# Optimization experiments

Measured on AMD Instinct MI355X. Metric: run time of the kernel, lower is better.

## Reference

```python
import jax, jax.numpy as jnp
import numpy as np

T, B, E = 1024, 4, 1024
H = 16
D = E // H          # head_dim = 64
L = 16              # max_relative_length


def setup_inputs() -> dict:
    key = jax.random.key(0)
    ks = jax.random.split(key, 4)
    query = jax.random.normal(ks[0], (T, B, E), dtype=jnp.float32)
    # xavier-ish scaled params
    in_proj_weight = jax.random.normal(ks[1], (3 * E, E), dtype=jnp.float32) * (1.0 / np.sqrt(E))
    in_proj_bias = jnp.zeros((3 * E,), dtype=jnp.float32)
    rel_pos_keys = jax.random.normal(ks[2], (2 * L + 1, E), dtype=jnp.float32) * (1.0 / np.sqrt(E))
    out_w = jax.random.normal(ks[3], (E, E), dtype=jnp.float32) * (1.0 / np.sqrt(E))
    out_b = jnp.zeros((E,), dtype=jnp.float32)
    return {"query": query, "in_proj_weight": in_proj_weight, "in_proj_bias": in_proj_bias,
            "rel_pos_keys": rel_pos_keys, "out_w": out_w, "out_b": out_b}


def reference(query, in_proj_weight, in_proj_bias, rel_pos_keys, out_w, out_b):
    t, b, e = query.shape
    scaling = D ** (-0.5)
    # fused qkv projection: [T,B,3E]
    qkv = jnp.einsum('tbe,fe->tbf', query, in_proj_weight) + in_proj_bias
    q, k, v = jnp.split(qkv, 3, axis=-1)
    q = q * scaling
    # [T,B,E] -> [B*H, T, D]
    def heads(x):
        return x.reshape(t, b * H, D).transpose(1, 0, 2)
    q, k, v = heads(q), heads(k), heads(v)
    # clipped relative position matrix [T,T] in [0, 2L]
    r = jnp.arange(t)
    dist = jnp.clip(r[None, :] - r[:, None], -L, L) + L
    # gather relation keys, keep first head_dim channels: [T,T,D]
    rel_k = rel_pos_keys[dist][:, :, :D]
    # scores = q k^T + q . rel_k  (Shaw et al.), [B*H, T, T]
    scores = jnp.einsum('btd,bsd->bts', q, k) + jnp.einsum('btd,tsd->bts', q, rel_k)
    probs = jax.nn.softmax(scores, axis=-1)
    attn = jnp.einsum('bts,bsd->btd', probs, v)      # [B*H, T, D]
    attn = attn.transpose(1, 0, 2).reshape(t, b, e)   # [T, B, E]
    return jnp.einsum('tbe,oe->tbo', attn, out_w) + out_b
```

## Files before the change

### kernel.cpp

```cpp
#include <hip/hip_runtime.h>

typedef __attribute__((ext_vector_type(8))) short short8;
typedef __attribute__((ext_vector_type(4))) float floatx4;


__device__ __forceinline__ short f2bf(float x) {
  union { float f; unsigned u; } cv; cv.f = x;
  unsigned u = cv.u + (0x7FFFu + ((cv.u >> 16) & 1u));
  return (short)(u >> 16);
}

__device__ __forceinline__ floatx4 mfma16(short8 a, short8 b, floatx4 c) {
  return __builtin_amdgcn_mfma_f32_16x16x32_bf16(a, b, c, 0, 0, 0);
}

__device__ __forceinline__ void async_copy16(const void* g, void* l) {
  __builtin_amdgcn_global_load_lds((const __attribute__((address_space(1))) void*)g,
                                   (__attribute__((address_space(3))) void*)l, 16, 0, 0);
}

__global__ void __launch_bounds__(256) f32_to_bf16_kernel(
    const float* __restrict__ src, short* __restrict__ dst, int n8)
{
  int i = blockIdx.x * 256 + threadIdx.x;
  if (i >= n8) return;
  const float4* s = (const float4*)src;
  float4 a = s[i * 2], b = s[i * 2 + 1];
  short8 o;
  o[0] = f2bf(a.x); o[1] = f2bf(a.y); o[2] = f2bf(a.z); o[3] = f2bf(a.w);
  o[4] = f2bf(b.x); o[5] = f2bf(b.y); o[6] = f2bf(b.z); o[7] = f2bf(b.w);
  *(short8*)(dst + (size_t)i * 8) = o;
}

__device__ __forceinline__ void gemm_core(
    const short* __restrict__ A, const short* __restrict__ W,
    short* Atile, short* Btile,
    int m0, int n0, int K, int tid, floatx4 acc[4][4])
{
  const int lane = tid & 63, w = tid >> 6;
  const int quad = lane >> 4, l16 = lane & 15;
  const int wm = (w >> 1) * 64, wn = (w & 1) * 64;
  #pragma unroll
  for (int mt = 0; mt < 4; mt++)
    #pragma unroll
    for (int nt = 0; nt < 4; nt++) acc[mt][nt] = (floatx4)(0.0f);

  for (int kk = 0; kk < K; kk += 32) {
    #pragma unroll
    for (int i = 0; i < 2; i++) {
      int seg = i * 256 + tid;
      int row = seg >> 2, c = seg & 3;
      const short* gA = A + (size_t)(m0 + row) * K + kk + c * 8;
      const short* gB = W + (size_t)(n0 + row) * K + kk + c * 8;
      async_copy16(gA, Atile + (size_t)(i * 256 + w * 64) * 8);
      async_copy16(gB, Btile + (size_t)(i * 256 + w * 64) * 8);
    }
    __syncthreads();
    short8 af[4], bfr[4];
    #pragma unroll
    for (int mt = 0; mt < 4; mt++)
      af[mt] = *(const short8*)(Atile + (wm + mt * 16 + l16) * 32 + quad * 8);
    #pragma unroll
    for (int nt = 0; nt < 4; nt++)
      bfr[nt] = *(const short8*)(Btile + (wn + nt * 16 + l16) * 32 + quad * 8);
    #pragma unroll
    for (int mt = 0; mt < 4; mt++)
      #pragma unroll
      for (int nt = 0; nt < 4; nt++)
        acc[mt][nt] = mfma16(af[mt], bfr[nt], acc[mt][nt]);
    __syncthreads();
  }
}

__global__ void __launch_bounds__(256) gemm_qkv(
    const short* __restrict__ A, const short* __restrict__ W,
    const float* __restrict__ bias,
    short* __restrict__ q_ws, short* __restrict__ k_ws, short* __restrict__ v_ws)
{
  __shared__ __align__(16) short Atile[128 * 32];
  __shared__ __align__(16) short Btile[128 * 32];
  const int tid = threadIdx.x;
  const int m0 = blockIdx.x * 128, n0 = blockIdx.y * 128;
  floatx4 acc[4][4];
  gemm_core(A, W, Atile, Btile, m0, n0, 1024, tid, acc);

  const int lane = tid & 63, w = tid >> 6;
  const int quad = lane >> 4, l16 = lane & 15;
  const int wm = (w >> 1) * 64, wn = (w & 1) * 64;
  #pragma unroll
  for (int nt = 0; nt < 4; nt++) {
    int f = n0 + wn + nt * 16 + l16;
    float bv = bias[f];
    int which = f >> 10;
    int h = (f >> 6) & 15;
    int d = f & 63;
    #pragma unroll
    for (int mt = 0; mt < 4; mt++) {
      #pragma unroll
      for (int reg = 0; reg < 4; reg++) {
        int r = m0 + wm + mt * 16 + quad * 4 + reg;
        int t = r >> 2, b = r & 3;
        int bh = b * 16 + h;
        float val = acc[mt][nt][reg] + bv;
        if (which == 0)      q_ws[((size_t)bh * 1024 + t) * 64 + d] = f2bf(val * 0.125f);
        else if (which == 1) k_ws[((size_t)bh * 1024 + t) * 64 + d] = f2bf(val);
        else                 v_ws[((size_t)bh * 64 + d) * 1024 + t] = f2bf(val);
      }
    }
  }
}

__global__ void __launch_bounds__(256) attn_kernel(
    const short* __restrict__ q_ws, const short* __restrict__ k_ws,
    const short* __restrict__ v_ws, const float* __restrict__ relk,
    short* __restrict__ attn_ws)
{
  __shared__ float rel_lds[64 * 33];
  __shared__ __align__(16) short Ktile[64 * 64];
  __shared__ __align__(16) short Vtile[64 * 64];
  __shared__ __align__(16) short p_lds[4][16 * 64];
  const int tid = threadIdx.x, lane = tid & 63, w = tid >> 6;
  const int quad = lane >> 4, l16 = lane & 15;
  const int bh = blockIdx.x >> 4;
  const int t0 = (blockIdx.x & 15) * 64;
  const int b = bh >> 4, h = bh & 15;

  short8 aq[2];
  #pragma unroll
  for (int ks = 0; ks < 2; ks++)
    aq[ks] = *(const short8*)(q_ws + ((size_t)bh * 1024 + t0 + w * 16 + l16) * 64
                              + ks * 32 + quad * 8);

  for (int i = tid; i < 48 * 8; i += 256) {
    int row = i >> 3, p = i & 7;
    short8 val;
    if (row < 33) {
      const float* src = relk + row * 1024 + p * 8;
      float4 a = *(const float4*)src, c = *(const float4*)(src + 4);
      val[0] = f2bf(a.x); val[1] = f2bf(a.y); val[2] = f2bf(a.z); val[3] = f2bf(a.w);
      val[4] = f2bf(c.x); val[5] = f2bf(c.y); val[6] = f2bf(c.z); val[7] = f2bf(c.w);
    } else {
      val = (short8)0;
    }
    *(short8*)(Ktile + row * 64 + ((p ^ (row & 7)) << 3)) = val;
  }
  __syncthreads();

  #pragma unroll
  for (int jt = 0; jt < 3; jt++) {
    floatx4 scR = (floatx4)(0.0f);
    #pragma unroll
    for (int ks = 0; ks < 2; ks++) {
      int rrow = jt * 16 + l16;
      int ck = (quad + 4 * ks) ^ (rrow & 7);
      short8 rb = *(const short8*)(Ktile + rrow * 64 + ck * 8);
      scR = mfma16(aq[ks], rb, scR);
    }
    int j = jt * 16 + l16;
    if (j < 33) {
      #pragma unroll
      for (int reg = 0; reg < 4; reg++) {
        int tl = w * 16 + quad * 4 + reg;
        rel_lds[tl * 33 + j] = scR[reg];
      }
    }
  }
  __syncthreads();

  floatx4 o[4];
  #pragma unroll
  for (int dt = 0; dt < 4; dt++) o[dt] = (floatx4)(0.0f);
  float rsum[4] = {0.f, 0.f, 0.f, 0.f};

  float biasLo[4], biasHi[4];
  #pragma unroll
  for (int reg = 0; reg < 4; reg++) {
    int tl = w * 16 + quad * 4 + reg;
    biasLo[reg] = rel_lds[tl * 33 + 0];
    biasHi[reg] = rel_lds[tl * 33 + 32];
  }

  const short* kg = k_ws + (size_t)bh * 1024 * 64;
  const short* vg = v_ws + (size_t)bh * 64 * 1024;

  for (int st = 0; st < 16; st++) {
    const int s0 = st * 64;
    #pragma unroll
    for (int i = 0; i < 2; i++) {
      int seg = i * 256 + tid;
      int row = seg >> 3, p = seg & 7;
      int ck = p ^ (row & 7);
      async_copy16(kg + (size_t)(s0 + row) * 64 + ck * 8,
                   Ktile + (size_t)(i * 256 + w * 64) * 8);
      async_copy16(vg + (size_t)row * 1024 + s0 + ck * 8,
                   Vtile + (size_t)(i * 256 + w * 64) * 8);
    }
    __syncthreads();

    floatx4 sc[4];
    #pragma unroll
    for (int nt = 0; nt < 4; nt++) {
      sc[nt] = (floatx4)(0.0f);
      #pragma unroll
      for (int ks = 0; ks < 2; ks++) {
        int srow = nt * 16 + l16;
        int ck = (quad + 4 * ks) ^ (l16 & 7);
        short8 kb = *(const short8*)(Ktile + srow * 64 + ck * 8);
        sc[nt] = mfma16(aq[ks], kb, sc[nt]);
      }
    }

    bool alllo = (s0 <= t0 + w * 16 - 79);
    bool allhi = (s0 >= t0 + w * 16 + 31);
    if (alllo || allhi) {
      #pragma unroll
      for (int reg = 0; reg < 4; reg++) {
        float bb = alllo ? biasLo[reg] : biasHi[reg];
        #pragma unroll
        for (int nt = 0; nt < 4; nt++) sc[nt][reg] += bb;
      }
    } else {
      #pragma unroll
      for (int nt = 0; nt < 4; nt++) {
        int s_glob = s0 + nt * 16 + l16;
        #pragma unroll
        for (int reg = 0; reg < 4; reg++) {
          int tl = w * 16 + quad * 4 + reg;
          int delta = min(max(s_glob - (t0 + tl), -16), 16) + 16;
          sc[nt][reg] += rel_lds[tl * 33 + delta];
        }
      }
    }

    #pragma unroll
    for (int nt = 0; nt < 4; nt++)
      #pragma unroll
      for (int reg = 0; reg < 4; reg++) {
        float p = __expf(sc[nt][reg]);
        sc[nt][reg] = p;
        rsum[reg] += p;
      }

    #pragma unroll
    for (int nt = 0; nt < 4; nt++)
      #pragma unroll
      for (int reg = 0; reg < 4; reg++) {
        int r = quad * 4 + reg;
        int cg = 2 * nt + (l16 >> 3);
        p_lds[w][r * 64 + ((cg ^ (r & 7)) << 3) + (l16 & 7)] = f2bf(sc[nt][reg]);
      }
    short8 ap[2];
    #pragma unroll
    for (int ks = 0; ks < 2; ks++) {
      int ck = (quad + 4 * ks) ^ (l16 & 7);
      ap[ks] = *(const short8*)(&p_lds[w][l16 * 64 + ck * 8]);
    }

    #pragma unroll
    for (int dt = 0; dt < 4; dt++) {
      #pragma unroll
      for (int ks = 0; ks < 2; ks++) {
        int drow = dt * 16 + l16;
        int ck = (quad + 4 * ks) ^ (l16 & 7);
        short8 vb = *(const short8*)(Vtile + drow * 64 + ck * 8);
        o[dt] = mfma16(ap[ks], vb, o[dt]);
      }
    }
    __syncthreads();
  }

  #pragma unroll
  for (int reg = 0; reg < 4; reg++) {
    float rs = rsum[reg];
    #pragma unroll
    for (int off = 1; off < 16; off <<= 1) rs += __shfl_xor(rs, off, 64);
    rsum[reg] = 1.0f / rs;
  }
  #pragma unroll
  for (int dt = 0; dt < 4; dt++) {
    #pragma unroll
    for (int reg = 0; reg < 4; reg++) {
      int tg = t0 + w * 16 + quad * 4 + reg;
      attn_ws[((size_t)tg * 4 + b) * 1024 + h * 64 + dt * 16 + l16]
        = f2bf(o[dt][reg] * rsum[reg]);
    }
  }
}

__global__ void __launch_bounds__(256) gemm_outproj(
    const short* __restrict__ A, const short* __restrict__ W,
    const float* __restrict__ bias, float* __restrict__ out)
{
  __shared__ __align__(16) short Atile[128 * 32];
  __shared__ __align__(16) short Btile[128 * 32];
  const int tid = threadIdx.x;
  const int m0 = blockIdx.x * 128, n0 = blockIdx.y * 128;
  floatx4 acc[4][4];
  gemm_core(A, W, Atile, Btile, m0, n0, 1024, tid, acc);

  const int lane = tid & 63, w = tid >> 6;
  const int quad = lane >> 4, l16 = lane & 15;
  const int wm = (w >> 1) * 64, wn = (w & 1) * 64;
  #pragma unroll
  for (int nt = 0; nt < 4; nt++) {
    int f = n0 + wn + nt * 16 + l16;
    float bv = bias[f];
    #pragma unroll
    for (int mt = 0; mt < 4; mt++) {
      #pragma unroll
      for (int reg = 0; reg < 4; reg++) {
        int r = m0 + wm + mt * 16 + quad * 4 + reg;
        out[(size_t)r * 1024 + f] = acc[mt][nt][reg] + bv;
      }
    }
  }
}

extern "C" void kernel_launch(void* const* d_in, const int* in_sizes, int n_in,
                              void* d_out, int out_size, void* d_ws, size_t ws_size,
                              hipStream_t stream) {
  const float* query = (const float*)d_in[0];
  const float* in_w  = (const float*)d_in[1];
  const float* in_b  = (const float*)d_in[2];
  const float* relk  = (const float*)d_in[3];
  const float* out_w = (const float*)d_in[4];
  const float* out_b = (const float*)d_in[5];
  float* out = (float*)d_out;

  short* qry_bf = (short*)d_ws;
  short* win_bf = qry_bf + (size_t)4096 * 1024;
  short* wout_bf = win_bf + (size_t)3072 * 1024;
  short* q_ws   = wout_bf + (size_t)1024 * 1024;
  short* k_ws   = q_ws + (size_t)64 * 1024 * 64;
  short* v_ws   = k_ws + (size_t)64 * 1024 * 64;
  short* att_ws = v_ws + (size_t)64 * 1024 * 64;

  f32_to_bf16_kernel<<<4096 * 1024 / 8 / 256, 256, 0, stream>>>(query, qry_bf, 4096 * 1024 / 8);
  f32_to_bf16_kernel<<<3072 * 1024 / 8 / 256, 256, 0, stream>>>(in_w, win_bf, 3072 * 1024 / 8);
  f32_to_bf16_kernel<<<1024 * 1024 / 8 / 256, 256, 0, stream>>>(out_w, wout_bf, 1024 * 1024 / 8);

  gemm_qkv<<<dim3(32, 24), 256, 0, stream>>>(qry_bf, win_bf, in_b, q_ws, k_ws, v_ws);
  attn_kernel<<<1024, 256, 0, stream>>>(q_ws, k_ws, v_ws, relk, att_ws);
  gemm_outproj<<<dim3(32, 8), 256, 0, stream>>>(att_ws, wout_bf, out_b, out);
}
```

Before: 198.0 us.

## Double-buffer LDS tiles in GEMMs and attention to overlap loads with MFMA

Splits the GEMM and attention K/V tile buffers into two LDS stages and issues the next tile's async global-to-LDS copy right after the barrier, before computing on the current tile. It also drops the trailing barrier in each loop. The goal is to hide global memory latency behind MFMA work. This doubles LDS use per block, which may reduce occupancy. Nothing explicitly waits for the async LDS loads (vmcnt) before the barrier, so correctness relies on how the barrier and the compiler order those loads.

```diff
diff --git a/kernel.cpp b/kernel.cpp
--- a/kernel.cpp
+++ b/kernel.cpp
@@ -32,9 +32,24 @@
   *(short8*)(dst + (size_t)i * 8) = o;
 }
 
-__device__ __forceinline__ void gemm_core(
+__device__ __forceinline__ void gemm_stage(
     const short* __restrict__ A, const short* __restrict__ W,
-    short* Atile, short* Btile,
+    short* Atile, short* Btile, int m0, int n0, int K, int kk, int tid, int w)
+{
+  #pragma unroll
+  for (int i = 0; i < 2; i++) {
+    int seg = i * 256 + tid;
+    int row = seg >> 2, c = seg & 3;
+    async_copy16(A + (size_t)(m0 + row) * K + kk + c * 8,
+                 Atile + (size_t)(i * 256 + w * 64) * 8);
+    async_copy16(W + (size_t)(n0 + row) * K + kk + c * 8,
+                 Btile + (size_t)(i * 256 + w * 64) * 8);
+  }
+}
+
+__device__ __forceinline__ void gemm_core_db(
+    const short* __restrict__ A, const short* __restrict__ W,
+    short* At, short* Bt,
     int m0, int n0, int K, int tid, floatx4 acc[4][4])
 {
   const int lane = tid & 63, w = tid >> 6;
@@ -45,30 +60,28 @@
     #pragma unroll
     for (int nt = 0; nt < 4; nt++) acc[mt][nt] = (floatx4)(0.0f);
 
+  gemm_stage(A, W, At, Bt, m0, n0, K, 0, tid, w);
+
   for (int kk = 0; kk < K; kk += 32) {
-    #pragma unroll
-    for (int i = 0; i < 2; i++) {
-      int seg = i * 256 + tid;
-      int row = seg >> 2, c = seg & 3;
-      const short* gA = A + (size_t)(m0 + row) * K + kk + c * 8;
-      const short* gB = W + (size_t)(n0 + row) * K + kk + c * 8;
-      async_copy16(gA, Atile + (size_t)(i * 256 + w * 64) * 8);
-      async_copy16(gB, Btile + (size_t)(i * 256 + w * 64) * 8);
-    }
+    const int cur = (kk >> 5) & 1;
+    short* Ac = At + cur * (128 * 32);
+    short* Bc = Bt + cur * (128 * 32);
     __syncthreads();
+    if (kk + 32 < K)
+      gemm_stage(A, W, At + (1 - cur) * (128 * 32), Bt + (1 - cur) * (128 * 32),
+                 m0, n0, K, kk + 32, tid, w);
     short8 af[4], bfr[4];
     #pragma unroll
     for (int mt = 0; mt < 4; mt++)
-      af[mt] = *(const short8*)(Atile + (wm + mt * 16 + l16) * 32 + quad * 8);
+      af[mt] = *(const short8*)(Ac + (wm + mt * 16 + l16) * 32 + quad * 8);
     #pragma unroll
     for (int nt = 0; nt < 4; nt++)
-      bfr[nt] = *(const short8*)(Btile + (wn + nt * 16 + l16) * 32 + quad * 8);
+      bfr[nt] = *(const short8*)(Bc + (wn + nt * 16 + l16) * 32 + quad * 8);
     #pragma unroll
     for (int mt = 0; mt < 4; mt++)
       #pragma unroll
       for (int nt = 0; nt < 4; nt++)
         acc[mt][nt] = mfma16(af[mt], bfr[nt], acc[mt][nt]);
-    __syncthreads();
   }
 }
 
@@ -77,12 +90,12 @@
     const float* __restrict__ bias,
     short* __restrict__ q_ws, short* __restrict__ k_ws, short* __restrict__ v_ws)
 {
-  __shared__ __align__(16) short Atile[128 * 32];
-  __shared__ __align__(16) short Btile[128 * 32];
+  __shared__ __align__(16) short Atile[2 * 128 * 32];
+  __shared__ __align__(16) short Btile[2 * 128 * 32];
   const int tid = threadIdx.x;
   const int m0 = blockIdx.x * 128, n0 = blockIdx.y * 128;
   floatx4 acc[4][4];
-  gemm_core(A, W, Atile, Btile, m0, n0, 1024, tid, acc);
+  gemm_core_db(A, W, Atile, Btile, m0, n0, 1024, tid, acc);
 
   const int lane = tid & 63, w = tid >> 6;
   const int quad = lane >> 4, l16 = lane & 15;
@@ -116,8 +129,8 @@
     short* __restrict__ attn_ws)
 {
   __shared__ float rel_lds[64 * 33];
-  __shared__ __align__(16) short Ktile[64 * 64];
-  __shared__ __align__(16) short Vtile[64 * 64];
+  __shared__ __align__(16) short Ktile[2][64 * 64];
+  __shared__ __align__(16) short Vtile[2][64 * 64];
   __shared__ __align__(16) short p_lds[4][16 * 64];
   const int tid = threadIdx.x, lane = tid & 63, w = tid >> 6;
   const int quad = lane >> 4, l16 = lane & 15;
@@ -142,7 +155,7 @@
     } else {
       val = (short8)0;
     }
-    *(short8*)(Ktile + row * 64 + ((p ^ (row & 7)) << 3)) = val;
+    *(short8*)(Ktile[0] + row * 64 + ((p ^ (row & 7)) << 3)) = val;
   }
   __syncthreads();
 
@@ -153,7 +166,7 @@
     for (int ks = 0; ks < 2; ks++) {
       int rrow = jt * 16 + l16;
       int ck = (quad + 4 * ks) ^ (rrow & 7);
-      short8 rb = *(const short8*)(Ktile + rrow * 64 + ck * 8);
+      short8 rb = *(const short8*)(Ktile[0] + rrow * 64 + ck * 8);
       scR = mfma16(aq[ks], rb, scR);
     }
     int j = jt * 16 + l16;
@@ -183,19 +196,27 @@
   const short* kg = k_ws + (size_t)bh * 1024 * 64;
   const short* vg = v_ws + (size_t)bh * 64 * 1024;
 
+  #define STAGE_KV(S0, BUF)                                                  \
+    {                                                                        \
+      _Pragma("unroll")                                                      \
+      for (int i = 0; i < 2; i++) {                                          \
+        int seg = i * 256 + tid;                                             \
+        int row = seg >> 3, p = seg & 7;                                     \
+        int ck = p ^ (row & 7);                                              \
+        async_copy16(kg + (size_t)((S0) + row) * 64 + ck * 8,                \
+                     Ktile[BUF] + (size_t)(i * 256 + w * 64) * 8);           \
+        async_copy16(vg + (size_t)row * 1024 + (S0) + ck * 8,                \
+                     Vtile[BUF] + (size_t)(i * 256 + w * 64) * 8);           \
+      }                                                                      \
+    }
+
+  STAGE_KV(0, 0);
+
   for (int st = 0; st < 16; st++) {
     const int s0 = st * 64;
-    #pragma unroll
-    for (int i = 0; i < 2; i++) {
-      int seg = i * 256 + tid;
-      int row = seg >> 3, p = seg & 7;
-      int ck = p ^ (row & 7);
-      async_copy16(kg + (size_t)(s0 + row) * 64 + ck * 8,
-                   Ktile + (size_t)(i * 256 + w * 64) * 8);
-      async_copy16(vg + (size_t)row * 1024 + s0 + ck * 8,
-                   Vtile + (size_t)(i * 256 + w * 64) * 8);
-    }
+    const int cur = st & 1;
     __syncthreads();
+    if (st < 15) STAGE_KV(s0 + 64, 1 - cur);
 
     floatx4 sc[4];
     #pragma unroll
@@ -205,7 +226,7 @@
       for (int ks = 0; ks < 2; ks++) {
         int srow = nt * 16 + l16;
         int ck = (quad + 4 * ks) ^ (l16 & 7);
-        short8 kb = *(const short8*)(Ktile + srow * 64 + ck * 8);
+        short8 kb = *(const short8*)(Ktile[cur] + srow * 64 + ck * 8);
         sc[nt] = mfma16(aq[ks], kb, sc[nt]);
       }
     }
@@ -262,12 +283,12 @@
       for (int ks = 0; ks < 2; ks++) {
         int drow = dt * 16 + l16;
         int ck = (quad + 4 * ks) ^ (l16 & 7);
-        short8 vb = *(const short8*)(Vtile + drow * 64 + ck * 8);
+        short8 vb = *(const short8*)(Vtile[cur] + drow * 64 + ck * 8);
         o[dt] = mfma16(ap[ks], vb, o[dt]);
       }
     }
-    __syncthreads();
-  }
+  }
+  #undef STAGE_KV
 
   #pragma unroll
   for (int reg = 0; reg < 4; reg++) {
@@ -291,12 +312,12 @@
     const short* __restrict__ A, const short* __restrict__ W,
     const float* __restrict__ bias, float* __restrict__ out)
 {
-  __shared__ __align__(16) short Atile[128 * 32];
-  __shared__ __align__(16) short Btile[128 * 32];
+  __shared__ __align__(16) short Atile[2 * 128 * 32];
+  __shared__ __align__(16) short Btile[2 * 128 * 32];
   const int tid = threadIdx.x;
   const int m0 = blockIdx.x * 128, n0 = blockIdx.y * 128;
   floatx4 acc[4][4];
-  gemm_core(A, W, Atile, Btile, m0, n0, 1024, tid, acc);
+  gemm_core_db(A, W, Atile, Btile, m0, n0, 1024, tid, acc);
 
   const int lane = tid & 63, w = tid >> 6;
   const int quad = lane >> 4, l16 = lane & 15;
```

Measured after the change: 195.0 us. Within noise of the previous version (-1.5%).
